# Performance work log

Measured on AMD Instinct MI355X. Metric: run time of the kernel, lower is better.

## Reference

```python
import jax, jax.numpy as jnp
import numpy as np
import math

N = 8192
FIN = 256
FOUT = 256


def setup_inputs() -> dict:
    key = jax.random.key(0)
    k1, k2, k3, k4 = jax.random.split(key, 4)
    x = jax.random.normal(k1, (N, FIN), dtype=jnp.float32)
    adj = jax.random.uniform(k2, (N, N), dtype=jnp.float32)
    stdv = 1.0 / math.sqrt(FOUT)
    W = jax.random.uniform(k3, (FIN, FOUT), minval=-stdv, maxval=stdv, dtype=jnp.float32)
    b = jax.random.uniform(k4, (FOUT,), minval=-stdv, maxval=stdv, dtype=jnp.float32)
    return {"input": x, "adj": adj, "W": W, "b": b}


def reference(input, adj, W, b):
    # add self-loops, then symmetric degree normalization: D^{-1/2} A D^{-1/2}
    A = adj + jnp.eye(adj.shape[0], dtype=adj.dtype)
    D = 1.0 / jnp.sqrt(jnp.sum(A, axis=1))          # [N]
    A = A * D[:, None] * D[None, :]                  # normalized adjacency [N, N]
    support = input @ W                              # [N, FOUT]
    out = A @ support                                # aggregation (dense equiv of sparse.mm)
    return jax.nn.relu(out + b)
```

## Files before the change

### kernel.cpp

```cpp
#include <hip/hip_runtime.h>
#include <hip/hip_bf16.h>

#define NROW 8192
#define FINC 256
#define FOUTC 256
#define BM 64
#define BK 64
#define KSPLIT 4
#define KLOC (NROW / KSPLIT)
#define NTL (KLOC / BK)

typedef __attribute__((ext_vector_type(8))) short bf16x8;
typedef __attribute__((ext_vector_type(4))) float f32x4;

__device__ __forceinline__ unsigned short f2bf(float f) {
  unsigned u = __float_as_uint(f);
  u += 0x7fffu + ((u >> 16) & 1u);
  return (unsigned short)(u >> 16);
}
__device__ __forceinline__ float bf2f(unsigned short h) {
  return __uint_as_float(((unsigned)h) << 16);
}

__global__ __launch_bounds__(256) void rowsum_kernel(const float* __restrict__ adj,
                                                     float* __restrict__ D) {
  const int row = blockIdx.x * 4 + (threadIdx.x >> 6);
  const int l = threadIdx.x & 63;
  const float4* p = reinterpret_cast<const float4*>(adj + (size_t)row * NROW);
  float s0 = 0.f, s1 = 0.f, s2 = 0.f, s3 = 0.f;
#pragma unroll
  for (int i = 0; i < 8; ++i) {
    float4 a = p[l + (i * 4 + 0) * 64];
    float4 b = p[l + (i * 4 + 1) * 64];
    float4 c = p[l + (i * 4 + 2) * 64];
    float4 d = p[l + (i * 4 + 3) * 64];
    s0 += (a.x + a.y) + (a.z + a.w);
    s1 += (b.x + b.y) + (b.z + b.w);
    s2 += (c.x + c.y) + (c.z + c.w);
    s3 += (d.x + d.y) + (d.z + d.w);
  }
  float s = (s0 + s1) + (s2 + s3);
#pragma unroll
  for (int off = 32; off > 0; off >>= 1) s += __shfl_down(s, off, 64);
  if (l == 0) D[row] = 1.0f / sqrtf(s + 1.0f);
}

__global__ __launch_bounds__(256) void support_kernel(const float* __restrict__ x,
                                                      const float* __restrict__ W,
                                                      const float* __restrict__ D,
                                                      unsigned short* __restrict__ s2T,
                                                      unsigned short* __restrict__ s2R) {
  __shared__ float xs[32][FINC];
  const int t = threadIdx.x;
  const int r0 = blockIdx.x * 32;
  {
    const float4* xg = reinterpret_cast<const float4*>(x + (size_t)r0 * FINC);
    float4* xl = reinterpret_cast<float4*>(&xs[0][0]);
#pragma unroll
    for (int i = 0; i < 8; ++i) xl[t + i * 256] = xg[t + i * 256];
  }
  __syncthreads();
  const int w = t >> 6, l = t & 63;
  float acc[8][4] = {};
  const float4* W4 = reinterpret_cast<const float4*>(W);
#pragma unroll 4
  for (int k = 0; k < FINC; ++k) {
    float4 wv = W4[k * 64 + l];
#pragma unroll
    for (int m = 0; m < 8; ++m) {
      float xv = xs[w * 8 + m][k];
      acc[m][0] = fmaf(xv, wv.x, acc[m][0]);
      acc[m][1] = fmaf(xv, wv.y, acc[m][1]);
      acc[m][2] = fmaf(xv, wv.z, acc[m][2]);
      acc[m][3] = fmaf(xv, wv.w, acc[m][3]);
    }
  }
#pragma unroll
  for (int m = 0; m < 8; ++m) {
    const int j = r0 + w * 8 + m;
    const float d = D[j];
    const int f0 = l * 4;
    ushort4 rv;
    rv.x = f2bf(d * acc[m][0]);
    rv.y = f2bf(d * acc[m][1]);
    rv.z = f2bf(d * acc[m][2]);
    rv.w = f2bf(d * acc[m][3]);
    *reinterpret_cast<ushort4*>(&s2R[(size_t)j * FOUTC + f0]) = rv;
    s2T[(size_t)(f0 + 0) * NROW + j] = rv.x;
    s2T[(size_t)(f0 + 1) * NROW + j] = rv.y;
    s2T[(size_t)(f0 + 2) * NROW + j] = rv.z;
    s2T[(size_t)(f0 + 3) * NROW + j] = rv.w;
  }
}

__global__ __launch_bounds__(512) void gcn_gemm_kernel(const float* __restrict__ adj,
                                                       const unsigned short* __restrict__ s2T,
                                                       float* __restrict__ part) {
  __shared__ __align__(16) unsigned short As[2][BM * BK];
  __shared__ __align__(16) unsigned short Bs[2][FOUTC * BK];

  const int t = threadIdx.x, wid = t >> 6, l = t & 63;
  const int bid = blockIdx.x;
  const int m = bid >> 2, ks = bid & 3;
  const int bm0 = m * BM;
  const size_t k0 = (size_t)ks * KLOC;

  const int ar = t >> 3, ac = t & 7;
  const float4* arow = reinterpret_cast<const float4*>(adj + (size_t)(bm0 + ar) * NROW + k0) + ac;
  const unsigned awoff0 = (unsigned)(ar * 128 + ((ac * 8) ^ ((ar & 7) << 4)));
  const unsigned awoff1 = (unsigned)(ar * 128 + ((ac * 8 + 64) ^ ((ar & 7) << 4)));

  const int bn = l >> 3;
  const unsigned bks = (unsigned)(((l & 7) * 16) ^ (bn << 4));

  f32x4 acc[2][4] = {};

  const int wm = wid >> 2, wn = wid & 3;
  const int am0 = wm * 32, nb0 = wn * 64;
  const unsigned swz = (unsigned)((l & 7) << 4);
  const int fr = l & 15;
  const unsigned kb = (unsigned)((l >> 4) * 16);

  auto stageB = [&](int kt, int sl) {
#pragma unroll
    for (int i = 0; i < 4; ++i) {
      const int c = wid * 4 + i;
      const int n = c * 8 + bn;
      const unsigned short* src = s2T + (size_t)n * NROW + k0 + (size_t)kt * BK;
      __builtin_amdgcn_global_load_lds(
          (const __attribute__((address_space(1))) unsigned int*)((const char*)src + bks),
          (__attribute__((address_space(3))) unsigned int*)((char*)&Bs[sl][0] + c * 1024),
          16, 0, 0);
    }
  };
  auto writeA = [&](float4 v0, float4 v1, int sl) {
    ushort4 u0, u1;
    u0.x = f2bf(v0.x); u0.y = f2bf(v0.y); u0.z = f2bf(v0.z); u0.w = f2bf(v0.w);
    u1.x = f2bf(v1.x); u1.y = f2bf(v1.y); u1.z = f2bf(v1.z); u1.w = f2bf(v1.w);
    *reinterpret_cast<ushort4*>((char*)&As[sl][0] + awoff0) = u0;
    *reinterpret_cast<ushort4*>((char*)&As[sl][0] + awoff1) = u1;
  };
  auto compute = [&](int sl) {
    const char* Ab = (const char*)&As[sl][0];
    const char* Bb = (const char*)&Bs[sl][0];
#pragma unroll
    for (int kk = 0; kk < 2; ++kk) {
      const unsigned kx = ((unsigned)(kk * 64) + kb) ^ swz;
      bf16x8 a0 = *reinterpret_cast<const bf16x8*>(Ab + (am0 + fr) * 128 + kx);
      bf16x8 a1 = *reinterpret_cast<const bf16x8*>(Ab + (am0 + 16 + fr) * 128 + kx);
      bf16x8 b0 = *reinterpret_cast<const bf16x8*>(Bb + (nb0 + fr) * 128 + kx);
      bf16x8 b1 = *reinterpret_cast<const bf16x8*>(Bb + (nb0 + 16 + fr) * 128 + kx);
      bf16x8 b2 = *reinterpret_cast<const bf16x8*>(Bb + (nb0 + 32 + fr) * 128 + kx);
      bf16x8 b3 = *reinterpret_cast<const bf16x8*>(Bb + (nb0 + 48 + fr) * 128 + kx);
      acc[0][0] = __builtin_amdgcn_mfma_f32_16x16x32_bf16(a0, b0, acc[0][0], 0, 0, 0);
      acc[0][1] = __builtin_amdgcn_mfma_f32_16x16x32_bf16(a0, b1, acc[0][1], 0, 0, 0);
      acc[0][2] = __builtin_amdgcn_mfma_f32_16x16x32_bf16(a0, b2, acc[0][2], 0, 0, 0);
      acc[0][3] = __builtin_amdgcn_mfma_f32_16x16x32_bf16(a0, b3, acc[0][3], 0, 0, 0);
      acc[1][0] = __builtin_amdgcn_mfma_f32_16x16x32_bf16(a1, b0, acc[1][0], 0, 0, 0);
      acc[1][1] = __builtin_amdgcn_mfma_f32_16x16x32_bf16(a1, b1, acc[1][1], 0, 0, 0);
      acc[1][2] = __builtin_amdgcn_mfma_f32_16x16x32_bf16(a1, b2, acc[1][2], 0, 0, 0);
      acc[1][3] = __builtin_amdgcn_mfma_f32_16x16x32_bf16(a1, b3, acc[1][3], 0, 0, 0);
    }
  };

  float4 aR0_0, aR0_1, aR1_0, aR1_1;
  {
    float4 v0 = arow[0], v1 = arow[8];
    asm volatile("s_waitcnt vmcnt(0)" ::: "memory");
    writeA(v0, v1, 0);
    stageB(0, 0);
    asm volatile("" ::: "memory");
    aR1_0 = arow[16]; aR1_1 = arow[24];
  }

#define GITER(T, SC, SN, AW0, AW1, AN0, AN1)                                   \
  asm volatile("s_waitcnt vmcnt(2) lgkmcnt(0)\n\ts_barrier" ::: "memory");     \
  stageB((T) + 1, SN);                                                         \
  asm volatile("" ::: "memory");                                               \
  AN0 = arow[((T) + 2) * 16]; AN1 = arow[((T) + 2) * 16 + 8];                  \
  compute(SC);                                                                 \
  asm volatile("s_waitcnt vmcnt(6)" ::: "memory");                             \
  writeA(AW0, AW1, SN);

#pragma unroll 1
  for (int tt = 0; tt < NTL - 2; tt += 2) {
    GITER(tt + 0, 0, 1, aR1_0, aR1_1, aR0_0, aR0_1)
    GITER(tt + 1, 1, 0, aR0_0, aR0_1, aR1_0, aR1_1)
  }
#undef GITER
  asm volatile("s_waitcnt vmcnt(2) lgkmcnt(0)\n\ts_barrier" ::: "memory");
  stageB(NTL - 1, 1);
  compute(0);
  asm volatile("s_waitcnt vmcnt(4)" ::: "memory");
  writeA(aR1_0, aR1_1, 1);
  asm volatile("s_waitcnt vmcnt(0) lgkmcnt(0)\n\ts_barrier" ::: "memory");
  compute(1);

  float* pout = part + (size_t)ks * NROW * FOUTC;
#pragma unroll
  for (int mm = 0; mm < 2; ++mm) {
#pragma unroll
    for (int n = 0; n < 4; ++n) {
#pragma unroll
      for (int q = 0; q < 4; ++q) {
        const int i = bm0 + am0 + mm * 16 + (l >> 4) * 4 + q;
        const int f = nb0 + n * 16 + fr;
        pout[(size_t)i * FOUTC + f] = acc[mm][n][q];
      }
    }
  }
}

__global__ __launch_bounds__(256) void combine_kernel(const float* __restrict__ part,
                                                      const unsigned short* __restrict__ s2R,
                                                      const float* __restrict__ D,
                                                      const float* __restrict__ bias,
                                                      float* __restrict__ out) {
  const int idx = blockIdx.x * 256 + threadIdx.x;
  const int i = idx >> 6;
  const int f0 = (idx & 63) * 4;
  const size_t off = (size_t)i * FOUTC + f0;
  const size_t stride = (size_t)NROW * FOUTC;
  float4 p0 = *reinterpret_cast<const float4*>(part + off);
  float4 p1 = *reinterpret_cast<const float4*>(part + stride + off);
  float4 p2 = *reinterpret_cast<const float4*>(part + 2 * stride + off);
  float4 p3 = *reinterpret_cast<const float4*>(part + 3 * stride + off);
  ushort4 sv = *reinterpret_cast<const ushort4*>(s2R + off);
  float di = D[i];
  float4 bv = *reinterpret_cast<const float4*>(bias + f0);
  float4 o;
  o.x = fmaxf((p0.x + p1.x + p2.x + p3.x + bf2f(sv.x)) * di + bv.x, 0.f);
  o.y = fmaxf((p0.y + p1.y + p2.y + p3.y + bf2f(sv.y)) * di + bv.y, 0.f);
  o.z = fmaxf((p0.z + p1.z + p2.z + p3.z + bf2f(sv.z)) * di + bv.z, 0.f);
  o.w = fmaxf((p0.w + p1.w + p2.w + p3.w + bf2f(sv.w)) * di + bv.w, 0.f);
  *reinterpret_cast<float4*>(out + off) = o;
}

__global__ __launch_bounds__(512) void gemm_fb(const float* __restrict__ adj,
                                               const unsigned short* __restrict__ s2T,
                                               const float* __restrict__ D,
                                               const float* __restrict__ bias,
                                               float* __restrict__ out) {
  __shared__ __align__(16) unsigned short As[3][32 * BK];
  __shared__ __align__(16) unsigned short Bs[3][FOUTC * BK];
  const int t = threadIdx.x, wid = t >> 6, l = t & 63;
  const int bm0 = blockIdx.x * 32;
  const int ar = t >> 4;
  const unsigned awoff = (unsigned)(ar * 128 + (((t & 15) * 8) ^ ((ar & 7) << 4)));
  const float4* arow = reinterpret_cast<const float4*>(adj + (size_t)(bm0 + ar) * NROW) + (t & 15);
  const int bn = l >> 3;
  const unsigned bks = (unsigned)(((l & 7) * 16) ^ (bn << 4));
  f32x4 acc[2][2] = {};
  const unsigned swz = (unsigned)((l & 7) << 4);
  const int fr = l & 15;
  const unsigned kb = (unsigned)((l >> 4) * 16);
  const int nb = wid * 32;
  const int NTF = NROW / BK;
  auto stageB = [&](int kt, int sl) {
#pragma unroll
    for (int i = 0; i < 4; ++i) {
      const int c = wid * 4 + i;
      const int n = c * 8 + bn;
      const unsigned short* src = s2T + (size_t)n * NROW + (size_t)kt * BK;
      __builtin_amdgcn_global_load_lds(
          (const __attribute__((address_space(1))) unsigned int*)((const char*)src + bks),
          (__attribute__((address_space(3))) unsigned int*)((char*)&Bs[sl][0] + c * 1024),
          16, 0, 0);
    }
  };
  auto writeA = [&](float4 av, int sl) {
    ushort4 ab;
    ab.x = f2bf(av.x); ab.y = f2bf(av.y); ab.z = f2bf(av.z); ab.w = f2bf(av.w);
    *reinterpret_cast<ushort4*>((char*)&As[sl][0] + awoff) = ab;
  };
  auto compute = [&](int sl) {
    const char* Ab = (const char*)&As[sl][0];
    const char* Bb = (const char*)&Bs[sl][0];
#pragma unroll
    for (int kk = 0; kk < 2; ++kk) {
      const unsigned kx = ((unsigned)(kk * 64) + kb) ^ swz;
      bf16x8 a0 = *reinterpret_cast<const bf16x8*>(Ab + fr * 128 + kx);
      bf16x8 a1 = *reinterpret_cast<const bf16x8*>(Ab + (fr + 16) * 128 + kx);
      bf16x8 b0 = *reinterpret_cast<const bf16x8*>(Bb + (nb + fr) * 128 + kx);
      bf16x8 b1 = *reinterpret_cast<const bf16x8*>(Bb + (nb + 16 + fr) * 128 + kx);
      acc[0][0] = __builtin_amdgcn_mfma_f32_16x16x32_bf16(a0, b0, acc[0][0], 0, 0, 0);
      acc[0][1] = __builtin_amdgcn_mfma_f32_16x16x32_bf16(a0, b1, acc[0][1], 0, 0, 0);
      acc[1][0] = __builtin_amdgcn_mfma_f32_16x16x32_bf16(a1, b0, acc[1][0], 0, 0, 0);
      acc[1][1] = __builtin_amdgcn_mfma_f32_16x16x32_bf16(a1, b1, acc[1][1], 0, 0, 0);
    }
  };
  float4 a0p, a1p, a2p;
  {
    float4 a0v = arow[0];
    asm volatile("" ::: "memory");
    stageB(0, 0);
    a1p = arow[16];
    asm volatile("" ::: "memory");
    stageB(1, 1);
    a2p = arow[32];
    asm volatile("s_waitcnt vmcnt(10)" ::: "memory");
    writeA(a0v, 0);
  }
#define PIPE_ITER(KT, S0, S1, S2, AW, AN)                                      \
  asm volatile("s_waitcnt vmcnt(5) lgkmcnt(0)\n\ts_barrier" ::: "memory");     \
  writeA(AW, S1);                                                              \
  stageB((KT) + 2, S2);                                                        \
  if ((KT) < NTF - 3) AN = arow[((KT) + 3) * 16];                              \
  compute(S0);
#pragma unroll 1
  for (int kt = 0; kt < NTF - 2; kt += 3) {
    PIPE_ITER(kt + 0, 0, 1, 2, a1p, a0p)
    PIPE_ITER(kt + 1, 1, 2, 0, a2p, a1p)
    PIPE_ITER(kt + 2, 2, 0, 1, a0p, a2p)
  }
#undef PIPE_ITER
  asm volatile("s_waitcnt vmcnt(4) lgkmcnt(0)\n\ts_barrier" ::: "memory");
  writeA(a1p, 1);
  compute(0);
  asm volatile("s_waitcnt vmcnt(0) lgkmcnt(0)\n\ts_barrier" ::: "memory");
  compute(1);
#pragma unroll
  for (int m = 0; m < 2; ++m) {
#pragma unroll
    for (int n = 0; n < 2; ++n) {
#pragma unroll
      for (int q = 0; q < 4; ++q) {
        const int i = bm0 + m * 16 + (l >> 4) * 4 + q;
        const int f = wid * 32 + n * 16 + fr;
        const float selfv = bf2f(s2T[(size_t)f * NROW + i]);
        float v = (acc[m][n][q] + selfv) * D[i] + bias[f];
        out[(size_t)i * FOUTC + f] = fmaxf(v, 0.0f);
      }
    }
  }
}

extern "C" void kernel_launch(void* const* d_in, const int* in_sizes, int n_in,
                              void* d_out, int out_size, void* d_ws, size_t ws_size,
                              hipStream_t stream) {
  const float* x   = (const float*)d_in[0];
  const float* adj = (const float*)d_in[1];
  const float* W   = (const float*)d_in[2];
  const float* b   = (const float*)d_in[3];
  float* out = (float*)d_out;

  char* wsb = (char*)d_ws;
  float* D            = (float*)wsb;
  unsigned short* s2T = (unsigned short*)(wsb + 32768);
  unsigned short* s2R = (unsigned short*)(wsb + 32768 + (1u << 22));
  float* part         = (float*)(wsb + 32768 + (2u << 22));

  const size_t need = 32768ull + (2ull << 22) + (size_t)KSPLIT * NROW * FOUTC * 4ull;
  rowsum_kernel<<<NROW / 4, 256, 0, stream>>>(adj, D);
  support_kernel<<<NROW / 32, 256, 0, stream>>>(x, W, D, s2T, s2R);
  if (ws_size >= need) {
    gcn_gemm_kernel<<<(NROW / BM) * KSPLIT, 512, 0, stream>>>(adj, s2T, part);
    combine_kernel<<<NROW * FOUTC / 1024, 256, 0, stream>>>(part, s2R, D, b, out);
  } else {
    gemm_fb<<<NROW / 32, 512, 0, stream>>>(adj, s2T, D, b, out);
  }
}
```

Before: 163.2 us.

## Halve K tile, double split-K, and restructure GEMM pipeline for higher occupancy

The main adjacency GEMM now uses a 32-wide K tile and an 8-way split-K instead of 64 and 4. Each block uses half the LDS and requests 6 blocks per CU, so more blocks run concurrently and latency is hidden by occupancy. The hand-scheduled waitcnt pipeline is replaced by a simpler double-buffered loop with __syncthreads, and half the threads convert and write A to alternate buffers. Partial output traffic doubles because the combine kernel now sums 8 partials, and barriers are more frequent.

```diff
diff --git a/kernel.cpp b/kernel.cpp
--- a/kernel.cpp
+++ b/kernel.cpp
@@ -5,8 +5,8 @@
 #define FINC 256
 #define FOUTC 256
 #define BM 64
-#define BK 64
-#define KSPLIT 4
+#define BK 32
+#define KSPLIT 8
 #define KLOC (NROW / KSPLIT)
 #define NTL (KLOC / BK)
 
@@ -93,108 +93,92 @@
   }
 }
 
-__global__ __launch_bounds__(512) void gcn_gemm_kernel(const float* __restrict__ adj,
-                                                       const unsigned short* __restrict__ s2T,
-                                                       float* __restrict__ part) {
+__global__ __launch_bounds__(512, 6) void gcn_gemm_kernel(const float* __restrict__ adj,
+                                                          const unsigned short* __restrict__ s2T,
+                                                          float* __restrict__ part) {
   __shared__ __align__(16) unsigned short As[2][BM * BK];
   __shared__ __align__(16) unsigned short Bs[2][FOUTC * BK];
 
   const int t = threadIdx.x, wid = t >> 6, l = t & 63;
   const int bid = blockIdx.x;
-  const int m = bid >> 2, ks = bid & 3;
+  const int m = bid >> 3, ks = bid & 7;
   const int bm0 = m * BM;
   const size_t k0 = (size_t)ks * KLOC;
 
   const int ar = t >> 3, ac = t & 7;
-  const float4* arow = reinterpret_cast<const float4*>(adj + (size_t)(bm0 + ar) * NROW + k0) + ac;
-  const unsigned awoff0 = (unsigned)(ar * 128 + ((ac * 8) ^ ((ar & 7) << 4)));
-  const unsigned awoff1 = (unsigned)(ar * 128 + ((ac * 8 + 64) ^ ((ar & 7) << 4)));
-
-  const int bn = l >> 3;
-  const unsigned bks = (unsigned)(((l & 7) * 16) ^ (bn << 4));
+  const float* aptr = adj + (size_t)(bm0 + ar) * NROW + k0 + ac * 8;
+  const unsigned awoff = (unsigned)(ar * 64 + (((ac & 3) ^ ((ar >> 1) & 3)) << 4));
+
+  const unsigned bsrc = (unsigned)(((l & 3) ^ ((l >> 3) & 3)) * 16);
+  const int brow = l >> 2;
 
   f32x4 acc[2][4] = {};
 
   const int wm = wid >> 2, wn = wid & 3;
   const int am0 = wm * 32, nb0 = wn * 64;
-  const unsigned swz = (unsigned)((l & 7) << 4);
   const int fr = l & 15;
-  const unsigned kb = (unsigned)((l >> 4) * 16);
+  const unsigned aroff = (unsigned)((am0 + fr) * 64 +
+                         ((((unsigned)(l >> 4)) ^ (((am0 + fr) >> 1) & 3)) << 4));
+  const unsigned broff = (unsigned)((nb0 + fr) * 64 +
+                         ((((unsigned)(l >> 4)) ^ (((nb0 + fr) >> 1) & 3)) << 4));
 
   auto stageB = [&](int kt, int sl) {
 #pragma unroll
-    for (int i = 0; i < 4; ++i) {
-      const int c = wid * 4 + i;
-      const int n = c * 8 + bn;
-      const unsigned short* src = s2T + (size_t)n * NROW + k0 + (size_t)kt * BK;
+    for (int i = 0; i < 2; ++i) {
+      const int c = wid * 2 + i;
+      const unsigned short* src =
+          s2T + (size_t)(c * 16 + brow) * NROW + k0 + (size_t)kt * BK;
       __builtin_amdgcn_global_load_lds(
-          (const __attribute__((address_space(1))) unsigned int*)((const char*)src + bks),
+          (const __attribute__((address_space(1))) unsigned int*)((const char*)src + bsrc),
           (__attribute__((address_space(3))) unsigned int*)((char*)&Bs[sl][0] + c * 1024),
           16, 0, 0);
     }
   };
-  auto writeA = [&](float4 v0, float4 v1, int sl) {
-    ushort4 u0, u1;
-    u0.x = f2bf(v0.x); u0.y = f2bf(v0.y); u0.z = f2bf(v0.z); u0.w = f2bf(v0.w);
-    u1.x = f2bf(v1.x); u1.y = f2bf(v1.y); u1.z = f2bf(v1.z); u1.w = f2bf(v1.w);
-    *reinterpret_cast<ushort4*>((char*)&As[sl][0] + awoff0) = u0;
-    *reinterpret_cast<ushort4*>((char*)&As[sl][0] + awoff1) = u1;
+  auto dsWriteA = [&](float4 v0, float4 v1, int sl) {
+    bf16x8 u;
+    u[0] = (short)f2bf(v0.x); u[1] = (short)f2bf(v0.y);
+    u[2] = (short)f2bf(v0.z); u[3] = (short)f2bf(v0.w);
+    u[4] = (short)f2bf(v1.x); u[5] = (short)f2bf(v1.y);
+    u[6] = (short)f2bf(v1.z); u[7] = (short)f2bf(v1.w);
+    *reinterpret_cast<bf16x8*>((char*)&As[sl][0] + awoff) = u;
   };
   auto compute = [&](int sl) {
     const char* Ab = (const char*)&As[sl][0];
     const char* Bb = (const char*)&Bs[sl][0];
-#pragma unroll
-    for (int kk = 0; kk < 2; ++kk) {
-      const unsigned kx = ((unsigned)(kk * 64) + kb) ^ swz;
-      bf16x8 a0 = *reinterpret_cast<const bf16x8*>(Ab + (am0 + fr) * 128 + kx);
-      bf16x8 a1 = *reinterpret_cast<const bf16x8*>(Ab + (am0 + 16 + fr) * 128 + kx);
-      bf16x8 b0 = *reinterpret_cast<const bf16x8*>(Bb + (nb0 + fr) * 128 + kx);
-      bf16x8 b1 = *reinterpret_cast<const bf16x8*>(Bb + (nb0 + 16 + fr) * 128 + kx);
-      bf16x8 b2 = *reinterpret_cast<const bf16x8*>(Bb + (nb0 + 32 + fr) * 128 + kx);
-      bf16x8 b3 = *reinterpret_cast<const bf16x8*>(Bb + (nb0 + 48 + fr) * 128 + kx);
-      acc[0][0] = __builtin_amdgcn_mfma_f32_16x16x32_bf16(a0, b0, acc[0][0], 0, 0, 0);
-      acc[0][1] = __builtin_amdgcn_mfma_f32_16x16x32_bf16(a0, b1, acc[0][1], 0, 0, 0);
-      acc[0][2] = __builtin_amdgcn_mfma_f32_16x16x32_bf16(a0, b2, acc[0][2], 0, 0, 0);
-      acc[0][3] = __builtin_amdgcn_mfma_f32_16x16x32_bf16(a0, b3, acc[0][3], 0, 0, 0);
-      acc[1][0] = __builtin_amdgcn_mfma_f32_16x16x32_bf16(a1, b0, acc[1][0], 0, 0, 0);
-      acc[1][1] = __builtin_amdgcn_mfma_f32_16x16x32_bf16(a1, b1, acc[1][1], 0, 0, 0);
-      acc[1][2] = __builtin_amdgcn_mfma_f32_16x16x32_bf16(a1, b2, acc[1][2], 0, 0, 0);
-      acc[1][3] = __builtin_amdgcn_mfma_f32_16x16x32_bf16(a1, b3, acc[1][3], 0, 0, 0);
-    }
-  };
-
-  float4 aR0_0, aR0_1, aR1_0, aR1_1;
-  {
-    float4 v0 = arow[0], v1 = arow[8];
-    asm volatile("s_waitcnt vmcnt(0)" ::: "memory");
-    writeA(v0, v1, 0);
-    stageB(0, 0);
-    asm volatile("" ::: "memory");
-    aR1_0 = arow[16]; aR1_1 = arow[24];
-  }
-
-#define GITER(T, SC, SN, AW0, AW1, AN0, AN1)                                   \
-  asm volatile("s_waitcnt vmcnt(2) lgkmcnt(0)\n\ts_barrier" ::: "memory");     \
-  stageB((T) + 1, SN);                                                         \
-  asm volatile("" ::: "memory");                                               \
-  AN0 = arow[((T) + 2) * 16]; AN1 = arow[((T) + 2) * 16 + 8];                  \
-  compute(SC);                                                                 \
-  asm volatile("s_waitcnt vmcnt(6)" ::: "memory");                             \
-  writeA(AW0, AW1, SN);
+    bf16x8 a0 = *reinterpret_cast<const bf16x8*>(Ab + aroff);
+    bf16x8 a1 = *reinterpret_cast<const bf16x8*>(Ab + aroff + 1024);
+#pragma unroll
+    for (int n = 0; n < 4; ++n) {
+      bf16x8 b = *reinterpret_cast<const bf16x8*>(Bb + broff + n * 1024);
+      acc[0][n] = __builtin_amdgcn_mfma_f32_16x16x32_bf16(a0, b, acc[0][n], 0, 0, 0);
+      acc[1][n] = __builtin_amdgcn_mfma_f32_16x16x32_bf16(a1, b, acc[1][n], 0, 0, 0);
+    }
+  };
+
+  float4 v0 = *reinterpret_cast<const float4*>(aptr);
+  float4 v1 = *reinterpret_cast<const float4*>(aptr + 4);
+  stageB(0, 0);
+  if (ac < 4) dsWriteA(v0, v1, 0);
+  __syncthreads();
 
 #pragma unroll 1
-  for (int tt = 0; tt < NTL - 2; tt += 2) {
-    GITER(tt + 0, 0, 1, aR1_0, aR1_1, aR0_0, aR0_1)
-    GITER(tt + 1, 1, 0, aR0_0, aR0_1, aR1_0, aR1_1)
-  }
-#undef GITER
-  asm volatile("s_waitcnt vmcnt(2) lgkmcnt(0)\n\ts_barrier" ::: "memory");
-  stageB(NTL - 1, 1);
-  compute(0);
-  asm volatile("s_waitcnt vmcnt(4)" ::: "memory");
-  writeA(aR1_0, aR1_1, 1);
-  asm volatile("s_waitcnt vmcnt(0) lgkmcnt(0)\n\ts_barrier" ::: "memory");
-  compute(1);
+  for (int tt = 0; tt < NTL; tt += 2) {
+    stageB(tt + 1, 1);
+    compute(0);
+    if (ac >= 4) dsWriteA(v0, v1, 1);
+    __syncthreads();
+    if (tt + 2 < NTL) {
+      float4 n0 = *reinterpret_cast<const float4*>(aptr + (tt + 2) * BK);
+      float4 n1 = *reinterpret_cast<const float4*>(aptr + (tt + 2) * BK + 4);
+      stageB(tt + 2, 0);
+      compute(1);
+      v0 = n0; v1 = n1;
+      if (ac < 4) dsWriteA(v0, v1, 0);
+    } else {
+      compute(1);
+    }
+    __syncthreads();
+  }
 
   float* pout = part + (size_t)ks * NROW * FOUTC;
 #pragma unroll
@@ -221,18 +205,20 @@
   const int f0 = (idx & 63) * 4;
   const size_t off = (size_t)i * FOUTC + f0;
   const size_t stride = (size_t)NROW * FOUTC;
-  float4 p0 = *reinterpret_cast<const float4*>(part + off);
-  float4 p1 = *reinterpret_cast<const float4*>(part + stride + off);
-  float4 p2 = *reinterpret_cast<const float4*>(part + 2 * stride + off);
-  float4 p3 = *reinterpret_cast<const float4*>(part + 3 * stride + off);
+  float4 s = *reinterpret_cast<const float4*>(part + off);
+#pragma unroll
+  for (int ks = 1; ks < KSPLIT; ++ks) {
+    float4 p = *reinterpret_cast<const float4*>(part + (size_t)ks * stride + off);
+    s.x += p.x; s.y += p.y; s.z += p.z; s.w += p.w;
+  }
   ushort4 sv = *reinterpret_cast<const ushort4*>(s2R + off);
   float di = D[i];
   float4 bv = *reinterpret_cast<const float4*>(bias + f0);
   float4 o;
-  o.x = fmaxf((p0.x + p1.x + p2.x + p3.x + bf2f(sv.x)) * di + bv.x, 0.f);
-  o.y = fmaxf((p0.y + p1.y + p2.y + p3.y + bf2f(sv.y)) * di + bv.y, 0.f);
-  o.z = fmaxf((p0.z + p1.z + p2.z + p3.z + bf2f(sv.z)) * di + bv.z, 0.f);
-  o.w = fmaxf((p0.w + p1.w + p2.w + p3.w + bf2f(sv.w)) * di + bv.w, 0.f);
+  o.x = fmaxf((s.x + bf2f(sv.x)) * di + bv.x, 0.f);
+  o.y = fmaxf((s.y + bf2f(sv.y)) * di + bv.y, 0.f);
+  o.z = fmaxf((s.z + bf2f(sv.z)) * di + bv.z, 0.f);
+  o.w = fmaxf((s.w + bf2f(sv.w)) * di + bv.w, 0.f);
   *reinterpret_cast<float4*>(out + off) = o;
 }
 
@@ -241,8 +227,8 @@
                                                const float* __restrict__ D,
                                                const float* __restrict__ bias,
                                                float* __restrict__ out) {
-  __shared__ __align__(16) unsigned short As[3][32 * BK];
-  __shared__ __align__(16) unsigned short Bs[3][FOUTC * BK];
+  __shared__ __align__(16) unsigned short Asf[3][32 * 64];
+  __shared__ __align__(16) unsigned short Bsf[3][FOUTC * 64];
   const int t = threadIdx.x, wid = t >> 6, l = t & 63;
   const int bm0 = blockIdx.x * 32;
   const int ar = t >> 4;
@@ -255,27 +241,27 @@
   const int fr = l & 15;
   const unsigned kb = (unsigned)((l >> 4) * 16);
   const int nb = wid * 32;
-  const int NTF = NROW / BK;
+  const int NTF = NROW / 64;
   auto stageB = [&](int kt, int sl) {
 #pragma unroll
     for (int i = 0; i < 4; ++i) {
       const int c = wid * 4 + i;
       const int n = c * 8 + bn;
-      const unsigned short* src = s2T + (size_t)n * NROW + (size_t)kt * BK;
+      const unsigned short* src = s2T + (size_t)n * NROW + (size_t)kt * 64;
       __builtin_amdgcn_global_load_lds(
           (const __attribute__((address_space(1))) unsigned int*)((const char*)src + bks),
-          (__attribute__((address_space(3))) unsigned int*)((char*)&Bs[sl][0] + c * 1024),
+          (__attribute__((address_space(3))) unsigned int*)((char*)&Bsf[sl][0] + c * 1024),
           16, 0, 0);
     }
   };
   auto writeA = [&](float4 av, int sl) {
     ushort4 ab;
     ab.x = f2bf(av.x); ab.y = f2bf(av.y); ab.z = f2bf(av.z); ab.w = f2bf(av.w);
-    *reinterpret_cast<ushort4*>((char*)&As[sl][0] + awoff) = ab;
+    *reinterpret_cast<ushort4*>((char*)&Asf[sl][0] + awoff) = ab;
   };
   auto compute = [&](int sl) {
-    const char* Ab = (const char*)&As[sl][0];
-    const char* Bb = (const char*)&Bs[sl][0];
+    const char* Ab = (const char*)&Asf[sl][0];
+    const char* Bb = (const char*)&Bsf[sl][0];
 #pragma unroll
     for (int kk = 0; kk < 2; ++kk) {
       const unsigned kx = ((unsigned)(kk * 64) + kb) ^ swz;
```

Measured after the change: 363.5 us. +122.8%, slower.

## Split output features across two blocks to raise occupancy in split-K GEMM

Applied to the files above, without the earlier changes.

Halves the N tile of the aggregation GEMM to 128 features, doubling the grid and cutting LDS and accumulator registers per block, with a bid remapping so paired feature-half blocks run close together and share adjacency tiles in cache. Wait counts are adjusted for the smaller B staging. The aim is more resident waves to hide memory latency, at the risk of the fp32 adjacency matrix being fetched twice from memory if cache reuse fails. The combine kernel is rewritten as a loop and the fallback LDS arrays are renamed.

```diff
diff --git a/kernel.cpp b/kernel.cpp
--- a/kernel.cpp
+++ b/kernel.cpp
@@ -5,6 +5,7 @@
 #define FINC 256
 #define FOUTC 256
 #define BM 64
+#define BN 128
 #define BK 64
 #define KSPLIT 4
 #define KLOC (NROW / KSPLIT)
@@ -93,15 +94,18 @@
   }
 }
 
-__global__ __launch_bounds__(512) void gcn_gemm_kernel(const float* __restrict__ adj,
-                                                       const unsigned short* __restrict__ s2T,
-                                                       float* __restrict__ part) {
+__global__ __launch_bounds__(512, 6) void gcn_gemm_kernel(const float* __restrict__ adj,
+                                                          const unsigned short* __restrict__ s2T,
+                                                          float* __restrict__ part) {
   __shared__ __align__(16) unsigned short As[2][BM * BK];
-  __shared__ __align__(16) unsigned short Bs[2][FOUTC * BK];
+  __shared__ __align__(16) unsigned short Bs[2][BN * BK];
 
   const int t = threadIdx.x, wid = t >> 6, l = t & 63;
   const int bid = blockIdx.x;
-  const int m = bid >> 2, ks = bid & 3;
+  const int x8 = bid & 7;
+  const int nh = (bid >> 3) & 1;
+  const int inner = (bid >> 4) * 8 + x8;
+  const int m = inner >> 2, ks = inner & 3;
   const int bm0 = m * BM;
   const size_t k0 = (size_t)ks * KLOC;
 
@@ -113,20 +117,20 @@
   const int bn = l >> 3;
   const unsigned bks = (unsigned)(((l & 7) * 16) ^ (bn << 4));
 
-  f32x4 acc[2][4] = {};
+  f32x4 acc[2][2] = {};
 
   const int wm = wid >> 2, wn = wid & 3;
-  const int am0 = wm * 32, nb0 = wn * 64;
+  const int am0 = wm * 32, nb0 = wn * 32;
   const unsigned swz = (unsigned)((l & 7) << 4);
   const int fr = l & 15;
   const unsigned kb = (unsigned)((l >> 4) * 16);
 
   auto stageB = [&](int kt, int sl) {
 #pragma unroll
-    for (int i = 0; i < 4; ++i) {
-      const int c = wid * 4 + i;
-      const int n = c * 8 + bn;
-      const unsigned short* src = s2T + (size_t)n * NROW + k0 + (size_t)kt * BK;
+    for (int i = 0; i < 2; ++i) {
+      const int c = wid * 2 + i;
+      const int frow = nh * BN + c * 8 + bn;
+      const unsigned short* src = s2T + (size_t)frow * NROW + k0 + (size_t)kt * BK;
       __builtin_amdgcn_global_load_lds(
           (const __attribute__((address_space(1))) unsigned int*)((const char*)src + bks),
           (__attribute__((address_space(3))) unsigned int*)((char*)&Bs[sl][0] + c * 1024),
@@ -150,16 +154,10 @@
       bf16x8 a1 = *reinterpret_cast<const bf16x8*>(Ab + (am0 + 16 + fr) * 128 + kx);
       bf16x8 b0 = *reinterpret_cast<const bf16x8*>(Bb + (nb0 + fr) * 128 + kx);
       bf16x8 b1 = *reinterpret_cast<const bf16x8*>(Bb + (nb0 + 16 + fr) * 128 + kx);
-      bf16x8 b2 = *reinterpret_cast<const bf16x8*>(Bb + (nb0 + 32 + fr) * 128 + kx);
-      bf16x8 b3 = *reinterpret_cast<const bf16x8*>(Bb + (nb0 + 48 + fr) * 128 + kx);
       acc[0][0] = __builtin_amdgcn_mfma_f32_16x16x32_bf16(a0, b0, acc[0][0], 0, 0, 0);
       acc[0][1] = __builtin_amdgcn_mfma_f32_16x16x32_bf16(a0, b1, acc[0][1], 0, 0, 0);
-      acc[0][2] = __builtin_amdgcn_mfma_f32_16x16x32_bf16(a0, b2, acc[0][2], 0, 0, 0);
-      acc[0][3] = __builtin_amdgcn_mfma_f32_16x16x32_bf16(a0, b3, acc[0][3], 0, 0, 0);
       acc[1][0] = __builtin_amdgcn_mfma_f32_16x16x32_bf16(a1, b0, acc[1][0], 0, 0, 0);
       acc[1][1] = __builtin_amdgcn_mfma_f32_16x16x32_bf16(a1, b1, acc[1][1], 0, 0, 0);
-      acc[1][2] = __builtin_amdgcn_mfma_f32_16x16x32_bf16(a1, b2, acc[1][2], 0, 0, 0);
-      acc[1][3] = __builtin_amdgcn_mfma_f32_16x16x32_bf16(a1, b3, acc[1][3], 0, 0, 0);
     }
   };
 
@@ -179,7 +177,7 @@
   asm volatile("" ::: "memory");                                               \
   AN0 = arow[((T) + 2) * 16]; AN1 = arow[((T) + 2) * 16 + 8];                  \
   compute(SC);                                                                 \
-  asm volatile("s_waitcnt vmcnt(6)" ::: "memory");                             \
+  asm volatile("s_waitcnt vmcnt(4)" ::: "memory");                             \
   writeA(AW0, AW1, SN);
 
 #pragma unroll 1
@@ -191,7 +189,7 @@
   asm volatile("s_waitcnt vmcnt(2) lgkmcnt(0)\n\ts_barrier" ::: "memory");
   stageB(NTL - 1, 1);
   compute(0);
-  asm volatile("s_waitcnt vmcnt(4)" ::: "memory");
+  asm volatile("s_waitcnt vmcnt(2)" ::: "memory");
   writeA(aR1_0, aR1_1, 1);
   asm volatile("s_waitcnt vmcnt(0) lgkmcnt(0)\n\ts_barrier" ::: "memory");
   compute(1);
@@ -200,11 +198,11 @@
 #pragma unroll
   for (int mm = 0; mm < 2; ++mm) {
 #pragma unroll
-    for (int n = 0; n < 4; ++n) {
+    for (int n = 0; n < 2; ++n) {
 #pragma unroll
       for (int q = 0; q < 4; ++q) {
         const int i = bm0 + am0 + mm * 16 + (l >> 4) * 4 + q;
-        const int f = nb0 + n * 16 + fr;
+        const int f = nh * BN + nb0 + n * 16 + fr;
         pout[(size_t)i * FOUTC + f] = acc[mm][n][q];
       }
     }
@@ -221,18 +219,20 @@
   const int f0 = (idx & 63) * 4;
   const size_t off = (size_t)i * FOUTC + f0;
   const size_t stride = (size_t)NROW * FOUTC;
-  float4 p0 = *reinterpret_cast<const float4*>(part + off);
-  float4 p1 = *reinterpret_cast<const float4*>(part + stride + off);
-  float4 p2 = *reinterpret_cast<const float4*>(part + 2 * stride + off);
-  float4 p3 = *reinterpret_cast<const float4*>(part + 3 * stride + off);
+  float4 s = *reinterpret_cast<const float4*>(part + off);
+#pragma unroll
+  for (int ks = 1; ks < KSPLIT; ++ks) {
+    float4 p = *reinterpret_cast<const float4*>(part + (size_t)ks * stride + off);
+    s.x += p.x; s.y += p.y; s.z += p.z; s.w += p.w;
+  }
   ushort4 sv = *reinterpret_cast<const ushort4*>(s2R + off);
   float di = D[i];
   float4 bv = *reinterpret_cast<const float4*>(bias + f0);
   float4 o;
-  o.x = fmaxf((p0.x + p1.x + p2.x + p3.x + bf2f(sv.x)) * di + bv.x, 0.f);
-  o.y = fmaxf((p0.y + p1.y + p2.y + p3.y + bf2f(sv.y)) * di + bv.y, 0.f);
-  o.z = fmaxf((p0.z + p1.z + p2.z + p3.z + bf2f(sv.z)) * di + bv.z, 0.f);
-  o.w = fmaxf((p0.w + p1.w + p2.w + p3.w + bf2f(sv.w)) * di + bv.w, 0.f);
+  o.x = fmaxf((s.x + bf2f(sv.x)) * di + bv.x, 0.f);
+  o.y = fmaxf((s.y + bf2f(sv.y)) * di + bv.y, 0.f);
+  o.z = fmaxf((s.z + bf2f(sv.z)) * di + bv.z, 0.f);
+  o.w = fmaxf((s.w + bf2f(sv.w)) * di + bv.w, 0.f);
   *reinterpret_cast<float4*>(out + off) = o;
 }
 
@@ -241,8 +241,8 @@
                                                const float* __restrict__ D,
                                                const float* __restrict__ bias,
                                                float* __restrict__ out) {
-  __shared__ __align__(16) unsigned short As[3][32 * BK];
-  __shared__ __align__(16) unsigned short Bs[3][FOUTC * BK];
+  __shared__ __align__(16) unsigned short Asf[3][32 * 64];
+  __shared__ __align__(16) unsigned short Bsf[3][FOUTC * 64];
   const int t = threadIdx.x, wid = t >> 6, l = t & 63;
   const int bm0 = blockIdx.x * 32;
   const int ar = t >> 4;
@@ -255,27 +255,27 @@
   const int fr = l & 15;
   const unsigned kb = (unsigned)((l >> 4) * 16);
   const int nb = wid * 32;
-  const int NTF = NROW / BK;
+  const int NTF = NROW / 64;
   auto stageB = [&](int kt, int sl) {
 #pragma unroll
     for (int i = 0; i < 4; ++i) {
       const int c = wid * 4 + i;
       const int n = c * 8 + bn;
-      const unsigned short* src = s2T + (size_t)n * NROW + (size_t)kt * BK;
+      const unsigned short* src = s2T + (size_t)n * NROW + (size_t)kt * 64;
       __builtin_amdgcn_global_load_lds(
           (const __attribute__((address_space(1))) unsigned int*)((const char*)src + bks),
-          (__attribute__((address_space(3))) unsigned int*)((char*)&Bs[sl][0] + c * 1024),
+          (__attribute__((address_space(3))) unsigned int*)((char*)&Bsf[sl][0] + c * 1024),
           16, 0, 0);
     }
   };
   auto writeA = [&](float4 av, int sl) {
     ushort4 ab;
     ab.x = f2bf(av.x); ab.y = f2bf(av.y); ab.z = f2bf(av.z); ab.w = f2bf(av.w);
-    *reinterpret_cast<ushort4*>((char*)&As[sl][0] + awoff) = ab;
+    *reinterpret_cast<ushort4*>((char*)&Asf[sl][0] + awoff) = ab;
   };
   auto compute = [&](int sl) {
-    const char* Ab = (const char*)&As[sl][0];
-    const char* Bb = (const char*)&Bs[sl][0];
+    const char* Ab = (const char*)&Asf[sl][0];
+    const char* Bb = (const char*)&Bsf[sl][0];
 #pragma unroll
     for (int kk = 0; kk < 2; ++kk) {
       const unsigned kx = ((unsigned)(kk * 64) + kb) ^ swz;
@@ -354,7 +354,7 @@
   rowsum_kernel<<<NROW / 4, 256, 0, stream>>>(adj, D);
   support_kernel<<<NROW / 32, 256, 0, stream>>>(x, W, D, s2T, s2R);
   if (ws_size >= need) {
-    gcn_gemm_kernel<<<(NROW / BM) * KSPLIT, 512, 0, stream>>>(adj, s2T, part);
+    gcn_gemm_kernel<<<(NROW / BM) * KSPLIT * 2, 512, 0, stream>>>(adj, s2T, part);
     combine_kernel<<<NROW * FOUTC / 1024, 256, 0, stream>>>(part, s2R, D, b, out);
   } else {
     gemm_fb<<<NROW / 32, 512, 0, stream>>>(adj, s2T, D, b, out);
```

Result: slower. 199.8 us (+22.4%).
